# Kernel optimization log

Hardware: AMD Instinct MI355X
Metric: run time of the kernel (lower is better)

## Reference

```python
import jax, jax.numpy as jnp
import numpy as np

MIN_FP16 = -65504.0  # torch.finfo(torch.float16).min
D_MODEL = 2048
NUM_HEAD = 16
HEAD_SIZE = D_MODEL // NUM_HEAD


def setup_inputs() -> dict:
    key = jax.random.key(0)
    k1, k2, k3, k4, k5 = jax.random.split(key, 5)
    B, S, D = 4, 2048, D_MODEL
    scale_in = 1.0 / np.sqrt(D)
    return {
        "x": jax.random.normal(k1, (B, S, D), dtype=jnp.float32),
        # nn.Linear(d_model, 3*d_model): weight [3D, D], bias [3D]
        "w_proj": jax.random.normal(k2, (3 * D, D), dtype=jnp.float32) * scale_in,
        "b_proj": jax.random.normal(k3, (3 * D,), dtype=jnp.float32) * 0.01,
        # nn.Linear(d_model, d_model)
        "w_ff": jax.random.normal(k4, (D, D), dtype=jnp.float32) * scale_in,
        "b_ff": jax.random.normal(k5, (D,), dtype=jnp.float32) * 0.01,
    }


def reference(x, w_proj, b_proj, w_ff, b_ff):
    B, S, D = x.shape
    H, hs = NUM_HEAD, HEAD_SIZE
    # fused QKV projection: [B,S,3D]
    x_proj = jnp.einsum("bsd,ed->bse", x, w_proj) + b_proj
    # view [B,S,H,3*hs] -> [B,H,S,3*hs], split into q,k,v [B,H,S,hs]
    x_proj = x_proj.reshape(B, S, H, 3 * hs).transpose(0, 2, 1, 3)
    q, k, v = jnp.split(x_proj, 3, axis=-1)
    next_prefix_kv = jnp.stack((k, v))  # [2,B,H,S,hs]
    # scaled scores [B,H,S,S]
    scores = jnp.einsum("bhqd,bhkd->bhqk", q, k) / np.sqrt(hs)
    # causal mask (prefix_kv=None => tmp_len == seq_len, offset 0)
    causal = jnp.tril(jnp.ones((S, S), dtype=bool))
    scores = jnp.where(causal, scores, MIN_FP16)
    probs = jax.nn.softmax(scores, axis=-1)  # dropout p=0 (eval)
    attn_o = jnp.einsum("bhqk,bhkd->bhqd", probs, v)
    attn_o = attn_o.transpose(0, 2, 1, 3).reshape(B, S, D)
    ff_o = jnp.einsum("bsd,ed->bse", attn_o, w_ff) + b_ff
    return ff_o, next_prefix_kv
```

## Files before the change

### kernel.cpp

```cpp
#include <hip/hip_runtime.h>


using floatx4 = __attribute__((ext_vector_type(4))) float;
using short8  = __attribute__((ext_vector_type(8))) short;

#define MFMA_BF16(a, b, c) __builtin_amdgcn_mfma_f32_16x16x32_bf16((a), (b), (c), 0, 0, 0)

static __device__ __forceinline__ unsigned short f2bf(float f) {
    unsigned u = __float_as_uint(f);
    u += 0x7FFF + ((u >> 16) & 1);
    return (unsigned short)(u >> 16);
}
static __device__ __forceinline__ short8 cvt8(const float* p) {
    float4 a = ((const float4*)p)[0];
    float4 b = ((const float4*)p)[1];
    short8 r;
    r[0] = (short)f2bf(a.x); r[1] = (short)f2bf(a.y);
    r[2] = (short)f2bf(a.z); r[3] = (short)f2bf(a.w);
    r[4] = (short)f2bf(b.x); r[5] = (short)f2bf(b.y);
    r[6] = (short)f2bf(b.z); r[7] = (short)f2bf(b.w);
    return r;
}

static __device__ __forceinline__ void gld16(const void* g, const void* l) {
    unsigned loff = (unsigned)__builtin_amdgcn_readfirstlane((int)(unsigned)(uintptr_t)l);
    __builtin_amdgcn_global_load_lds(
        (__attribute__((address_space(1))) unsigned*)(uintptr_t)g,
        (__attribute__((address_space(3))) unsigned*)loff,
        16, 0, 0);
}

__global__ __launch_bounds__(256) void cvt_kernel(
    const float* __restrict__ X, const float* __restrict__ Wp,
    const float* __restrict__ Wf,
    unsigned short* __restrict__ Xb, unsigned short* __restrict__ Wpb,
    unsigned short* __restrict__ Wfb, int doWf)
{
    const int NX = 2097152;
    const int NP = 1572864;
    const int NF = 524288;
    const int total = NX + NP + (doWf ? NF : 0);
    const int stride = gridDim.x * 256;
    for (int g = blockIdx.x * 256 + threadIdx.x; g < total; g += stride) {
        const float* src; unsigned short* dst; int off;
        if (g < NX)           { src = X;  dst = Xb;  off = g; }
        else if (g < NX + NP) { src = Wp; dst = Wpb; off = g - NX; }
        else                  { src = Wf; dst = Wfb; off = g - NX - NP; }
        short8 v = cvt8(src + (size_t)off * 8);
        *(short8*)(dst + (size_t)off * 8) = v;
    }
}

__global__ __launch_bounds__(256) void gemm_qkv_kernel(
    const unsigned short* __restrict__ Xb,
    const unsigned short* __restrict__ Wpb,
    const float* __restrict__ Bias,
    unsigned short* __restrict__ Qws,
    float* __restrict__ KV)
{
    const int K = 2048;
    __shared__ unsigned short As[128 * 64];
    __shared__ unsigned short Bs[128 * 64];
    const int n0 = blockIdx.x * 128;
    const int m0 = blockIdx.y * 128;
    const int t = threadIdx.x;
    const int w = t >> 6, l = t & 63;
    const int lr = l & 15, lq = l >> 4;
    const int wr = w >> 1, wc = w & 1;
    const int srow = l >> 3;
    const int scol = (l & 7) * 8;

    floatx4 acc[4][4];
#pragma unroll
    for (int mi = 0; mi < 4; ++mi)
#pragma unroll
        for (int ni = 0; ni < 4; ++ni) acc[mi][ni] = (floatx4){0, 0, 0, 0};

    for (int k0 = 0; k0 < K; k0 += 64) {
        __syncthreads();
#pragma unroll
        for (int i = 0; i < 4; ++i) {
            const int rb = (i * 4 + w) * 8;
            gld16(Xb  + (size_t)(m0 + rb + srow) * K + k0 + scol, &As[(rb)*64]);
            gld16(Wpb + (size_t)(n0 + rb + srow) * K + k0 + scol, &Bs[(rb)*64]);
        }
        __syncthreads();
#pragma unroll
        for (int kc = 0; kc < 2; ++kc) {
            short8 af[4], bg[4];
#pragma unroll
            for (int mi = 0; mi < 4; ++mi)
                af[mi] = *(const short8*)&As[(wr * 64 + mi * 16 + lr) * 64 + kc * 32 + lq * 8];
#pragma unroll
            for (int ni = 0; ni < 4; ++ni)
                bg[ni] = *(const short8*)&Bs[(wc * 64 + ni * 16 + lr) * 64 + kc * 32 + lq * 8];
#pragma unroll
            for (int mi = 0; mi < 4; ++mi)
#pragma unroll
                for (int ni = 0; ni < 4; ++ni)
                    acc[mi][ni] = MFMA_BF16(af[mi], bg[ni], acc[mi][ni]);
        }
    }
#pragma unroll
    for (int ni = 0; ni < 4; ++ni) {
        int e = n0 + wc * 64 + ni * 16 + lr;
        int h = e / 384;
        int c = e - h * 384;
        float bias = Bias[e];
#pragma unroll
        for (int mi = 0; mi < 4; ++mi) {
#pragma unroll
            for (int r = 0; r < 4; ++r) {
                int m = m0 + wr * 64 + mi * 16 + lq * 4 + r;
                int b = m >> 11, s = m & 2047;
                float o = acc[mi][ni][r] + bias;
                size_t base = (((size_t)(b * 16 + h)) * 2048 + s) * 128;
                if (c < 128)      Qws[base + c] = f2bf(o);
                else if (c < 256) KV[base + (c - 128)] = o;
                else              KV[(size_t)16777216 + base + (c - 256)] = o;
            }
        }
    }
}

__global__ __launch_bounds__(256) void repack_kv_kernel(
    const float* __restrict__ KV,
    unsigned short* __restrict__ Kb,
    unsigned short* __restrict__ Vtb)
{
    __shared__ short Vt[128][72];
    const int bh = blockIdx.x >> 5;
    const int w  = blockIdx.x & 31;
    const int t  = threadIdx.x;

    {
        const int kr = t >> 2;
        const int c4 = (t & 3) * 4;
        const int s  = w * 64 + kr;
        const float* kp = KV + ((size_t)bh * 2048 + s) * 128 + c4 * 8;
        unsigned short* ko = Kb + ((size_t)bh * 2048 + s) * 128;
        const int sw = s & 7;
#pragma unroll
        for (int j = 0; j < 4; ++j) {
            short8 v = cvt8(kp + j * 8);
            *(short8*)(ko + ((c4 + j) ^ sw) * 8) = v;
        }
    }

    {
        const int vkp = t & 31;
        const int vd0 = (t >> 5) * 16;
        const float* vap = KV + (((size_t)64 + bh) * 2048 + w * 64 + 2 * vkp) * 128 + vd0;
        short8 va0 = cvt8(vap),       va1 = cvt8(vap + 8);
        short8 vb0 = cvt8(vap + 128), vb1 = cvt8(vap + 136);
#pragma unroll
        for (int dd = 0; dd < 8; ++dd) {
            unsigned w0 = (unsigned)(unsigned short)va0[dd] |
                          ((unsigned)(unsigned short)vb0[dd] << 16);
            unsigned w1 = (unsigned)(unsigned short)va1[dd] |
                          ((unsigned)(unsigned short)vb1[dd] << 16);
            *(unsigned*)&Vt[vd0 + dd][2 * vkp]     = w0;
            *(unsigned*)&Vt[vd0 + 8 + dd][2 * vkp] = w1;
        }
    }
    __syncthreads();
    {
        const int d = t >> 1, hf = t & 1;
        unsigned short* vo = Vtb + ((size_t)bh * 128 + d) * 2048 + w * 64;
        const int dw = d & 7;
#pragma unroll
        for (int j = 0; j < 4; ++j) {
            int c = hf * 4 + j;
            uint4 v = *(const uint4*)&Vt[d][c * 8];
            *(uint4*)(vo + (c ^ dw) * 8) = v;
        }
    }
}

__global__ __launch_bounds__(256) void attn_kernel(
    unsigned short* __restrict__ QA,
    const unsigned short* __restrict__ Kb,
    const unsigned short* __restrict__ Vtb)
{
    const int S = 2048;
    __shared__ unsigned short Ks[64 * 128];
    __shared__ unsigned short Vt[128 * 64];
    __shared__ short Pb[4][16][72];

    const int bh = blockIdx.y;
    const int qt = gridDim.x - 1 - blockIdx.x;
    const int q0 = qt * 64;
    const int t = threadIdx.x;
    const int wv = t >> 6;
    const int l = t & 63;
    const int lr = l & 15;
    const int lq = l >> 4;
    const int lr7 = lr & 7;

    unsigned short* Qp = QA + ((size_t)bh * S + q0) * 128;
    const unsigned short* gK = Kb + (size_t)bh * S * 128;
    const unsigned short* gV = Vtb + (size_t)bh * 128 * S;

    short8 qf[4];
#pragma unroll
    for (int kc = 0; kc < 4; ++kc)
        qf[kc] = *(const short8*)(Qp + (size_t)(wv * 16 + lr) * 128 + kc * 32 + lq * 8);

    float m_i = -1e30f, l_i = 0.0f;
    floatx4 oacc[8];
#pragma unroll
    for (int nt = 0; nt < 8; ++nt) oacc[nt] = (floatx4){0, 0, 0, 0};

    const int ntiles = qt + 1;
    for (int it = 0; it < ntiles; ++it) {
        const int kv0 = it * 64;
        __syncthreads();
#pragma unroll
        for (int i = 0; i < 4; ++i) {
            const int off = (i * 16 + wv * 4) * 128;
            gld16(gK + (size_t)kv0 * 128 + off + l * 8, &Ks[off]);
        }
#pragma unroll
        for (int i = 0; i < 4; ++i) {
            const int ob = (i * 16 + wv * 4) * 256 + l * 16;
            const int d = ob >> 7, rem = ob & 127;
            gld16((const char*)gV + (size_t)d * (S * 2) + kv0 * 2 + rem,
                  (const char*)Vt + (i * 16 + wv * 4) * 256);
        }
        __syncthreads();

        floatx4 sacc[4];
#pragma unroll
        for (int mt = 0; mt < 4; ++mt) sacc[mt] = (floatx4){0, 0, 0, 0};
#pragma unroll
        for (int kc = 0; kc < 4; ++kc) {
#pragma unroll
            for (int mt = 0; mt < 4; ++mt) {
                short8 a = *(const short8*)
                    &Ks[(mt * 16 + lr) * 128 + ((((kc << 2) | lq) ^ lr7) << 3)];
                sacc[mt] = MFMA_BF16(a, qf[kc], sacc[mt]);
            }
        }

        float sv[16];
        const bool diag = (it == qt);
#pragma unroll
        for (int mt = 0; mt < 4; ++mt)
#pragma unroll
            for (int r = 0; r < 4; ++r) {
                float x = sacc[mt][r] * 0.08838834764831845f;
                if (diag && (mt * 16 + lq * 4 + r > wv * 16 + lr)) x = -1e30f;
                sv[mt * 4 + r] = x;
            }
        float mx = sv[0];
#pragma unroll
        for (int j = 1; j < 16; ++j) mx = fmaxf(mx, sv[j]);
        mx = fmaxf(mx, __shfl_xor(mx, 16));
        mx = fmaxf(mx, __shfl_xor(mx, 32));
        float m_new = fmaxf(m_i, mx);
        float alpha = __expf(m_i - m_new);
        m_i = m_new;
        float sum = 0.0f;
        unsigned pw[8];
#pragma unroll
        for (int j = 0; j < 8; ++j) {
            float p0 = __expf(sv[2 * j]     - m_new);
            float p1 = __expf(sv[2 * j + 1] - m_new);
            sum += p0 + p1;
            pw[j] = (unsigned)f2bf(p0) | ((unsigned)f2bf(p1) << 16);
        }
        sum += __shfl_xor(sum, 16);
        sum += __shfl_xor(sum, 32);
        l_i = l_i * alpha + sum;

#pragma unroll
        for (int mt = 0; mt < 4; ++mt)
            *(uint2*)&Pb[wv][lr][mt * 16 + lq * 4] =
                make_uint2(pw[2 * mt], pw[2 * mt + 1]);

        float am[4];
#pragma unroll
        for (int r = 0; r < 4; ++r) am[r] = __shfl(alpha, lq * 4 + r);
#pragma unroll
        for (int nt = 0; nt < 8; ++nt)
#pragma unroll
            for (int r = 0; r < 4; ++r) oacc[nt][r] *= am[r];

        short8 pa0 = *(const short8*)&Pb[wv][lr][lq * 8];
        short8 pa1 = *(const short8*)&Pb[wv][lr][32 + lq * 8];
#pragma unroll
        for (int nt = 0; nt < 8; ++nt) {
            const int row = nt * 16 + lr;
            short8 v0 = *(const short8*)&Vt[row * 64 + ((lq ^ lr7) << 3)];
            short8 v1 = *(const short8*)&Vt[row * 64 + (((4 + lq) ^ lr7) << 3)];
            oacc[nt] = MFMA_BF16(pa0, v0, oacc[nt]);
            oacc[nt] = MFMA_BF16(pa1, v1, oacc[nt]);
        }
    }

    float lm[4];
#pragma unroll
    for (int r = 0; r < 4; ++r) lm[r] = 1.0f / __shfl(l_i, lq * 4 + r);
#pragma unroll
    for (int nt = 0; nt < 8; ++nt) {
#pragma unroll
        for (int r = 0; r < 4; ++r) {
            int q = wv * 16 + lq * 4 + r;
            Qp[(size_t)q * 128 + nt * 16 + lr] = f2bf(oacc[nt][r] * lm[r]);
        }
    }
}

__global__ __launch_bounds__(256) void gemm_ff_kernel(
    const unsigned short* __restrict__ AOhm,
    const unsigned short* __restrict__ Wfb,
    const float* __restrict__ Bias,
    float* __restrict__ Out)
{
    const int K = 2048;
    __shared__ unsigned short As[128 * 64];
    __shared__ unsigned short Bs[128 * 64];
    const int n0 = blockIdx.x * 128;
    const int m0 = blockIdx.y * 128;
    const int t = threadIdx.x;
    const int w = t >> 6, l = t & 63;
    const int lr = l & 15, lq = l >> 4;
    const int wr = w >> 1, wc = w & 1;
    const int srow = l >> 3;
    const int scol = (l & 7) * 8;

    floatx4 acc[4][4];
#pragma unroll
    for (int mi = 0; mi < 4; ++mi)
#pragma unroll
        for (int ni = 0; ni < 4; ++ni) acc[mi][ni] = (floatx4){0, 0, 0, 0};

    for (int k0 = 0; k0 < K; k0 += 64) {
        const int h = k0 >> 7, d0 = (k0 & 127) + scol;
        __syncthreads();
#pragma unroll
        for (int i = 0; i < 4; ++i) {
            const int rb = (i * 4 + w) * 8;
            const int m = m0 + rb + srow;
            const int b = m >> 11, s = m & 2047;
            gld16(AOhm + ((size_t)(b * 16 + h) * 2048 + s) * 128 + d0, &As[(rb)*64]);
            gld16(Wfb  + (size_t)(n0 + rb + srow) * K + k0 + scol,     &Bs[(rb)*64]);
        }
        __syncthreads();
#pragma unroll
        for (int kc = 0; kc < 2; ++kc) {
            short8 af[4], bg[4];
#pragma unroll
            for (int mi = 0; mi < 4; ++mi)
                af[mi] = *(const short8*)&As[(wr * 64 + mi * 16 + lr) * 64 + kc * 32 + lq * 8];
#pragma unroll
            for (int ni = 0; ni < 4; ++ni)
                bg[ni] = *(const short8*)&Bs[(wc * 64 + ni * 16 + lr) * 64 + kc * 32 + lq * 8];
#pragma unroll
            for (int mi = 0; mi < 4; ++mi)
#pragma unroll
                for (int ni = 0; ni < 4; ++ni)
                    acc[mi][ni] = MFMA_BF16(af[mi], bg[ni], acc[mi][ni]);
        }
    }
#pragma unroll
    for (int ni = 0; ni < 4; ++ni) {
        int e = n0 + wc * 64 + ni * 16 + lr;
        float bias = Bias[e];
#pragma unroll
        for (int mi = 0; mi < 4; ++mi) {
#pragma unroll
            for (int r = 0; r < 4; ++r) {
                int m = m0 + wr * 64 + mi * 16 + lq * 4 + r;
                Out[(size_t)m * 2048 + e] = acc[mi][ni][r] + bias;
            }
        }
    }
}

__global__ __launch_bounds__(256) void gemm_ff_fb_kernel(
    const unsigned short* __restrict__ AOhm,
    const float* __restrict__ W,
    const float* __restrict__ Bias,
    float* __restrict__ Out)
{
    const int K = 2048;
    __shared__ short As[64][72];
    __shared__ short Bs[64][72];
    const int n0 = blockIdx.x * 64;
    const int m0 = blockIdx.y * 64;
    const int t = threadIdx.x;
    const int wv = t >> 6;
    const int l = t & 63;
    const int lr = l & 15;
    const int lq = l >> 4;
    const int srow = t >> 2;
    const int scol = (t & 3) << 4;

    floatx4 acc[4] = {{0,0,0,0},{0,0,0,0},{0,0,0,0},{0,0,0,0}};

    const int mrow = m0 + srow;
    const int b = mrow >> 11, s = mrow & 2047;
    const unsigned short* gA = AOhm + (size_t)(b * 16) * 262144 + (size_t)s * 128;
    const float* gB = W + (size_t)(n0 + srow) * K + scol;

    for (int k0 = 0; k0 < K; k0 += 64) {
        int kk = k0 + scol;
        int h = kk >> 7, d = kk & 127;
        const unsigned short* pa = gA + (size_t)h * 262144 + d;
        uint4 av0 = *(const uint4*)(pa);
        uint4 av1 = *(const uint4*)(pa + 8);
        short8 b0 = cvt8(gB + k0);
        short8 b1 = cvt8(gB + k0 + 8);
        __syncthreads();
        *(uint4*)&As[srow][scol]      = av0;
        *(uint4*)&As[srow][scol + 8]  = av1;
        *(short8*)&Bs[srow][scol]     = b0;
        *(short8*)&Bs[srow][scol + 8] = b1;
        __syncthreads();
#pragma unroll
        for (int kc = 0; kc < 2; ++kc) {
            short8 a = *(const short8*)&As[wv * 16 + lr][kc * 32 + lq * 8];
#pragma unroll
            for (int j = 0; j < 4; ++j) {
                short8 b2 = *(const short8*)&Bs[j * 16 + lr][kc * 32 + lq * 8];
                acc[j] = MFMA_BF16(a, b2, acc[j]);
            }
        }
    }
#pragma unroll
    for (int j = 0; j < 4; ++j) {
        int e = n0 + j * 16 + lr;
        float bias = Bias[e];
#pragma unroll
        for (int r = 0; r < 4; ++r) {
            int m = m0 + wv * 16 + lq * 4 + r;
            Out[(size_t)m * 2048 + e] = acc[j][r] + bias;
        }
    }
}

extern "C" void kernel_launch(void* const* d_in, const int* in_sizes, int n_in,
                              void* d_out, int out_size, void* d_ws, size_t ws_size,
                              hipStream_t stream) {
    const float* X  = (const float*)d_in[0];
    const float* Wp = (const float*)d_in[1];
    const float* bp = (const float*)d_in[2];
    const float* Wf = (const float*)d_in[3];
    const float* bf = (const float*)d_in[4];

    float* out = (float*)d_out;
    float* kv  = out + 16777216;
    unsigned short* Qws = (unsigned short*)d_ws;

    unsigned short* Xb  = (unsigned short*)out;
    unsigned short* Wpb = Xb + 16777216;
    unsigned short* Kbs = (unsigned short*)out;
    unsigned short* Vtb = Kbs + 16777216;
    const bool wfInWs = ws_size >= (size_t)33554432 + 8388608;
    unsigned short* Wfb = wfInWs ? Qws + 16777216 : (unsigned short*)nullptr;

    cvt_kernel<<<dim3(2048), 256, 0, stream>>>(X, Wp, Wf, Xb, Wpb, Wfb,
                                               wfInWs ? 1 : 0);
    gemm_qkv_kernel<<<dim3(48, 64), 256, 0, stream>>>(Xb, Wpb, bp, Qws, kv);
    repack_kv_kernel<<<dim3(2048), 256, 0, stream>>>(kv, Kbs, Vtb);
    attn_kernel<<<dim3(32, 64), 256, 0, stream>>>(Qws, Kbs, Vtb);
    if (wfInWs)
        gemm_ff_kernel<<<dim3(16, 64), 256, 0, stream>>>(Qws, Wfb, bf, out);
    else
        gemm_ff_fb_kernel<<<dim3(32, 128), 256, 0, stream>>>(Qws, Wf, bf, out);
}
```

Baseline: 972.6 us.

## Apply XOR swizzle to bf16 global layouts to remove LDS bank conflicts

Stores the converted bf16 operands (X, Wp, Wf) and the Q/attention-output workspace with 16-byte chunks XOR-permuted by row index. Because the gld16 copies move data straight into LDS, the LDS tiles end up swizzled, and the MFMA fragment reads can use XOR addressing that avoids bank conflicts without padding. The producers and consumers of that layout (QKV GEMM epilogue, attention Q load and output store, FF GEMM A loads) change together, so the scheme only works while every index stays consistent.

```diff
diff --git a/kernel.cpp b/kernel.cpp
--- a/kernel.cpp
+++ b/kernel.cpp
@@ -46,8 +46,11 @@
         if (g < NX)           { src = X;  dst = Xb;  off = g; }
         else if (g < NX + NP) { src = Wp; dst = Wpb; off = g - NX; }
         else                  { src = Wf; dst = Wfb; off = g - NX - NP; }
+        const int row = off >> 8;
+        const int c   = off & 255;
+        const int dof = (row << 8) | (c & ~7) | ((c ^ row) & 7);
         short8 v = cvt8(src + (size_t)off * 8);
-        *(short8*)(dst + (size_t)off * 8) = v;
+        *(short8*)(dst + (size_t)dof * 8) = v;
     }
 }
 
@@ -66,6 +69,7 @@
     const int t = threadIdx.x;
     const int w = t >> 6, l = t & 63;
     const int lr = l & 15, lq = l >> 4;
+    const int lr7 = lr & 7;
     const int wr = w >> 1, wc = w & 1;
     const int srow = l >> 3;
     const int scol = (l & 7) * 8;
@@ -90,10 +94,12 @@
             short8 af[4], bg[4];
 #pragma unroll
             for (int mi = 0; mi < 4; ++mi)
-                af[mi] = *(const short8*)&As[(wr * 64 + mi * 16 + lr) * 64 + kc * 32 + lq * 8];
+                af[mi] = *(const short8*)
+                    &As[(wr * 64 + mi * 16 + lr) * 64 + ((((kc << 2) | lq) ^ lr7) << 3)];
 #pragma unroll
             for (int ni = 0; ni < 4; ++ni)
-                bg[ni] = *(const short8*)&Bs[(wc * 64 + ni * 16 + lr) * 64 + kc * 32 + lq * 8];
+                bg[ni] = *(const short8*)
+                    &Bs[(wc * 64 + ni * 16 + lr) * 64 + ((((kc << 2) | lq) ^ lr7) << 3)];
 #pragma unroll
             for (int mi = 0; mi < 4; ++mi)
 #pragma unroll
@@ -115,7 +121,8 @@
                 int b = m >> 11, s = m & 2047;
                 float o = acc[mi][ni][r] + bias;
                 size_t base = (((size_t)(b * 16 + h)) * 2048 + s) * 128;
-                if (c < 128)      Qws[base + c] = f2bf(o);
+                if (c < 128)
+                    Qws[base + ((((c >> 3) ^ (s & 7)) << 3) | (c & 7))] = f2bf(o);
                 else if (c < 256) KV[base + (c - 128)] = o;
                 else              KV[(size_t)16777216 + base + (c - 256)] = o;
             }
@@ -204,7 +211,8 @@
     short8 qf[4];
 #pragma unroll
     for (int kc = 0; kc < 4; ++kc)
-        qf[kc] = *(const short8*)(Qp + (size_t)(wv * 16 + lr) * 128 + kc * 32 + lq * 8);
+        qf[kc] = *(const short8*)(Qp + (size_t)(wv * 16 + lr) * 128 +
+                                  ((((kc << 2) | lq) ^ lr7) << 3));
 
     float m_i = -1e30f, l_i = 0.0f;
     floatx4 oacc[8];
@@ -306,7 +314,8 @@
 #pragma unroll
         for (int r = 0; r < 4; ++r) {
             int q = wv * 16 + lq * 4 + r;
-            Qp[(size_t)q * 128 + nt * 16 + lr] = f2bf(oacc[nt][r] * lm[r]);
+            int ch = (nt * 2 + (lr >> 3)) ^ (q & 7);
+            Qp[(size_t)q * 128 + (ch << 3) + (lr & 7)] = f2bf(oacc[nt][r] * lm[r]);
         }
     }
 }
@@ -325,6 +334,7 @@
     const int t = threadIdx.x;
     const int w = t >> 6, l = t & 63;
     const int lr = l & 15, lq = l >> 4;
+    const int lr7 = lr & 7;
     const int wr = w >> 1, wc = w & 1;
     const int srow = l >> 3;
     const int scol = (l & 7) * 8;
@@ -352,10 +362,12 @@
             short8 af[4], bg[4];
 #pragma unroll
             for (int mi = 0; mi < 4; ++mi)
-                af[mi] = *(const short8*)&As[(wr * 64 + mi * 16 + lr) * 64 + kc * 32 + lq * 8];
+                af[mi] = *(const short8*)
+                    &As[(wr * 64 + mi * 16 + lr) * 64 + ((((kc << 2) | lq) ^ lr7) << 3)];
 #pragma unroll
             for (int ni = 0; ni < 4; ++ni)
-                bg[ni] = *(const short8*)&Bs[(wc * 64 + ni * 16 + lr) * 64 + kc * 32 + lq * 8];
+                bg[ni] = *(const short8*)
+                    &Bs[(wc * 64 + ni * 16 + lr) * 64 + ((((kc << 2) | lq) ^ lr7) << 3)];
 #pragma unroll
             for (int mi = 0; mi < 4; ++mi)
 #pragma unroll
@@ -401,15 +413,18 @@
 
     const int mrow = m0 + srow;
     const int b = mrow >> 11, s = mrow & 2047;
+    const int sw = s & 7;
     const unsigned short* gA = AOhm + (size_t)(b * 16) * 262144 + (size_t)s * 128;
     const float* gB = W + (size_t)(n0 + srow) * K + scol;
 
     for (int k0 = 0; k0 < K; k0 += 64) {
         int kk = k0 + scol;
         int h = kk >> 7, d = kk & 127;
-        const unsigned short* pa = gA + (size_t)h * 262144 + d;
-        uint4 av0 = *(const uint4*)(pa);
-        uint4 av1 = *(const uint4*)(pa + 8);
+        int span = (d >> 6) * 64;
+        int c0 = (d >> 3) & 7;
+        const unsigned short* pa = gA + (size_t)h * 262144 + span;
+        uint4 av0 = *(const uint4*)(pa + ((c0 ^ sw) << 3));
+        uint4 av1 = *(const uint4*)(pa + (((c0 + 1) ^ sw) << 3));
         short8 b0 = cvt8(gB + k0);
         short8 b1 = cvt8(gB + k0 + 8);
         __syncthreads();
```

Result: slower. 1.091 ms (+12.2%).
